# Optimization experiments

Hardware: AMD Instinct MI355X
Metric: run time of the kernel (lower is better)

The kernel has to match this reference:

```python
import jax, jax.numpy as jnp
import numpy as np

N_TOPICS = 1024
TOPIC_DIM = 128
HIDDEN = 512
N_HEADS = 8
HEAD_DIM = HIDDEN // N_HEADS
N_LAYERS = 2
ALPHA = 0.2
TIME_DECAY = 0.1
BATCH = 8


def setup_inputs() -> dict:
    key = jax.random.key(0)
    ks = jax.random.split(key, 16)
    inp = {
        'topic_ids': jax.random.randint(ks[0], (BATCH,), 0, N_TOPICS, dtype=jnp.int32),
        'adj_matrix': jax.random.randint(ks[1], (BATCH, N_TOPICS, N_TOPICS), 0, 2, dtype=jnp.int32),
        'time_matrix': jax.random.uniform(ks[2], (BATCH, N_TOPICS, N_TOPICS), dtype=jnp.float32),
        'attractiveness': jax.random.normal(ks[3], (BATCH,), dtype=jnp.float32),
        # parameters (torch Linear convention: W [out,in], y = x@W.T + b)
        'topic_embedding': jax.random.normal(ks[4], (N_TOPICS, TOPIC_DIM), dtype=jnp.float32) * 0.1,
        'struct_W': jax.random.normal(ks[5], (HIDDEN, TOPIC_DIM), dtype=jnp.float32) * 0.05,
        'struct_b': jnp.zeros((HIDDEN,), dtype=jnp.float32),
        'attract_W': jax.random.normal(ks[6], (HIDDEN, 1), dtype=jnp.float32) * 0.05,
        'attract_b': jnp.zeros((HIDDEN,), dtype=jnp.float32),
        'gat_W': jax.random.normal(ks[7], (N_LAYERS, N_HEADS, HIDDEN, HEAD_DIM), dtype=jnp.float32) * 0.05,
        'gat_a': jax.random.normal(ks[8], (N_LAYERS, N_HEADS, 2 * HEAD_DIM, 1), dtype=jnp.float32) * 0.05,
        'fc1_W': jax.random.normal(ks[9], (HIDDEN, HIDDEN), dtype=jnp.float32) * 0.05,
        'fc1_b': jnp.zeros((HIDDEN,), dtype=jnp.float32),
        'fc2_W': jax.random.normal(ks[10], (1, HIDDEN), dtype=jnp.float32) * 0.05,
        'fc2_b': jnp.zeros((1,), dtype=jnp.float32),
    }
    return inp


def _gat_layer(node, adj, time_w, W, a):
    # node: [B,N,F], adj: [B,N,N] (0/1), time_w: [B,N,N]
    # W: [H,F,hd], a: [H,2*hd,1]
    h = jnp.einsum('bni,hio->bhno', node, W)  # [B,H,N,hd]
    # Additive attention: a = [a_src; a_dst] so e_ij = LeakyReLU(h_i.a_src + h_j.a_dst)
    a_src = a[:, :HEAD_DIM, 0]   # [H,hd]
    a_dst = a[:, HEAD_DIM:, 0]   # [H,hd]
    e_src = jnp.einsum('bhnd,hd->bhn', h, a_src)  # [B,H,N]
    e_dst = jnp.einsum('bhnd,hd->bhn', h, a_dst)  # [B,H,N]
    e = e_src[:, :, :, None] + e_dst[:, :, None, :]  # [B,H,N,N]
    e = jax.nn.leaky_relu(e, negative_slope=ALPHA)
    e = e * time_w[:, None, :, :]
    e = jnp.where(adj[:, None, :, :] == 0, -jnp.inf, e)
    attn = jax.nn.softmax(e, axis=-1)
    out = jnp.einsum('bhij,bhjd->bhid', attn, h)  # [B,H,N,hd]
    out = out.transpose(0, 2, 1, 3).reshape(node.shape[0], node.shape[1], -1)
    return jax.nn.elu(out)


def reference(topic_ids, adj_matrix, time_matrix, attractiveness,
              topic_embedding, struct_W, struct_b, attract_W, attract_b,
              gat_W, gat_a, fc1_W, fc1_b, fc2_W, fc2_b):
    # structural features for all topics -> hidden
    struct = topic_embedding @ struct_W.T + struct_b          # [N,hidden]
    attract = attractiveness[:, None] @ attract_W.T + attract_b  # [B,hidden]
    node = jnp.broadcast_to(struct[None], (BATCH, N_TOPICS, HIDDEN))
    # weighted co-occurrence time (eq.17)
    time_w = jnp.exp(-TIME_DECAY * (time_matrix.max() - time_matrix))  # [B,N,N]
    for l in range(N_LAYERS):
        node = _gat_layer(node, adj_matrix, time_w, gat_W[l], gat_a[l])
    # gather per-sample topic node feature
    topic_feat = jnp.take_along_axis(node, topic_ids[:, None, None].astype(jnp.int32), axis=1)[:, 0]  # [B,hidden]
    combined = topic_feat + attract
    hidden = jax.nn.relu(combined @ fc1_W.T + fc1_b)
    pred = hidden @ fc2_W.T + fc2_b  # [B,1]
    return pred
```

## Files before the change

### kernel.cpp

```cpp
#include <hip/hip_runtime.h>

#define NT 1024
#define TD 128
#define HID 512
#define NH 8
#define HD 64
#define NB 8

typedef unsigned short us;
typedef _Float16 h16;
typedef h16 half8 __attribute__((ext_vector_type(8)));
typedef h16 h16x2 __attribute__((ext_vector_type(2)));
typedef float f32x4 __attribute__((ext_vector_type(4)));

#define LOG2E 1.44269504f

extern "C" __device__ _Float16 __ocml_exp2_f16(_Float16);

__device__ __forceinline__ us f2h(float x) { return __builtin_bit_cast(us, (h16)x); }
__device__ __forceinline__ float h2f(us s) { return (float)__builtin_bit_cast(h16, s); }
__device__ __forceinline__ unsigned int pkh2(float a, float b) {
    auto v = __builtin_amdgcn_cvt_pkrtz(a, b);
    return __builtin_bit_cast(unsigned int, v);
}

__global__ __launch_bounds__(256) void kprep(const float* __restrict__ tm, float* __restrict__ part,
                                             const float* __restrict__ emb, const float* __restrict__ sW,
                                             const float* __restrict__ sb, us* __restrict__ node0b,
                                             const float* __restrict__ gW, us* __restrict__ Wt,
                                             const float* __restrict__ fc2b, float* __restrict__ out) {
    __shared__ __align__(16) float smf[8768];
    int bx = blockIdx.x, t = threadIdx.x;
    if (bx < 1024) {
        const float4* tm4 = (const float4*)tm;
        size_t base = (size_t)bx * 256 + t;
        float m = -1e30f;
        #pragma unroll
        for (int k = 0; k < 8; k++) {
            float4 v = tm4[base + (size_t)k * 262144];
            m = fmaxf(m, fmaxf(fmaxf(v.x, v.y), fmaxf(v.z, v.w)));
        }
        smf[t] = m; __syncthreads();
        for (int s = 128; s > 0; s >>= 1) { if (t < s) smf[t] = fmaxf(smf[t], smf[t + s]); __syncthreads(); }
        if (t == 0) part[bx] = smf[0];
    } else if (bx < 1152) {
        int g = bx - 1024; int iblk = g & 15, oseg = g >> 4;
        us* As = (us*)smf;
        us* Bs = (us*)smf + 64 * 136;
        const float4* esrc = (const float4*)(emb + (size_t)iblk * 64 * TD);
        const float4* wsrc = (const float4*)(sW + (size_t)oseg * 64 * TD);
        #pragma unroll
        for (int rep = 0; rep < 8; rep++) {
            int f = rep * 256 + t;
            int row = f >> 5, c4 = f & 31;
            float4 av = esrc[f];
            float4 bv = wsrc[f];
            uint2 pa, pb;
            pa.x = pkh2(av.x, av.y); pa.y = pkh2(av.z, av.w);
            pb.x = pkh2(bv.x, bv.y); pb.y = pkh2(bv.z, bv.w);
            *(uint2*)&As[row * 136 + c4 * 4] = pa;
            *(uint2*)&Bs[row * 136 + c4 * 4] = pb;
        }
        __syncthreads();
        int l = t & 63, w = t >> 6, m = l & 15, q = l >> 4;
        f32x4 acc[4];
        #pragma unroll
        for (int ot = 0; ot < 4; ot++) acc[ot] = (f32x4){0.f, 0.f, 0.f, 0.f};
        #pragma unroll
        for (int ks = 0; ks < 4; ks++) {
            half8 a = *(const half8*)&As[(w * 16 + m) * 136 + ks * 32 + q * 8];
            #pragma unroll
            for (int ot = 0; ot < 4; ot++) {
                half8 b = *(const half8*)&Bs[(ot * 16 + m) * 136 + ks * 32 + q * 8];
                acc[ot] = __builtin_amdgcn_mfma_f32_16x16x32_f16(a, b, acc[ot], 0, 0, 0);
            }
        }
        #pragma unroll
        for (int ot = 0; ot < 4; ot++) {
            int col = oseg * 64 + ot * 16 + m;
            float sbv = sb[col];
            #pragma unroll
            for (int rr = 0; rr < 4; rr++) {
                int rowi = iblk * 64 + w * 16 + q * 4 + rr;
                node0b[(size_t)rowi * HID + col] = f2h(acc[ot][rr] + sbv);
            }
        }
    } else {
        int g = bx - 1152; int lh = g >> 3, kt = g & 7;
        if (g == 0 && t < NB) out[t] = fc2b[0];
        float* tile = smf;
        const float4* src = (const float4*)(gW + ((size_t)lh * HID + kt * 64) * HD);
        #pragma unroll
        for (int rep = 0; rep < 4; rep++) {
            int f = rep * 256 + t;
            float4 v = src[f];
            int row = f >> 4, col = (f & 15) * 4;
            float* d = tile + row * 65 + col;
            d[0] = v.x; d[1] = v.y; d[2] = v.z; d[3] = v.w;
        }
        __syncthreads();
        int o = t >> 2, ks = (t & 3) * 16;
        us pk[16];
        #pragma unroll
        for (int j = 0; j < 16; j++) pk[j] = f2h(tile[(ks + j) * 65 + o]);
        us* dst = Wt + (size_t)lh * HD * HID + (size_t)o * HID + kt * 64 + ks;
        *(uint4*)dst = *(uint4*)pk;
        *(uint4*)(dst + 8) = *(uint4*)&pk[8];
    }
}

__device__ __forceinline__ void gemm_body(const us* __restrict__ A, const us* __restrict__ W,
                                          const float* __restrict__ gav,
                                          us* __restrict__ outT, us* __restrict__ outR,
                                          float* __restrict__ esO, float* __restrict__ edO,
                                          int iblk, int b, int h, int t, us* sm) {
    us* As = sm;
    us* Bs = sm + 2 * 4608;
    int row = t >> 2, ks = t & 3;
    int l = t & 63, w = t >> 6, m = l & 15, q = l >> 4;
    size_t arow0 = (size_t)(b * NT + iblk * 64);
    const us* ar = A + (arow0 + row) * HID + ks * 16;
    const us* br = W + ((size_t)(h * HD + row)) * HID + ks * 16;
    f32x4 acc[4];
    #pragma unroll
    for (int ot = 0; ot < 4; ot++) acc[ot] = (f32x4){0.f, 0.f, 0.f, 0.f};
    {
        uint4 x0 = *(const uint4*)ar, x1 = *(const uint4*)(ar + 8);
        uint4 y0 = *(const uint4*)br, y1 = *(const uint4*)(br + 8);
        *(uint4*)&As[row * 72 + ks * 16] = x0; *(uint4*)&As[row * 72 + ks * 16 + 8] = x1;
        *(uint4*)&Bs[row * 72 + ks * 16] = y0; *(uint4*)&Bs[row * 72 + ks * 16 + 8] = y1;
    }
    uint4 a0 = *(const uint4*)(ar + 64), a1 = *(const uint4*)(ar + 72);
    uint4 b0 = *(const uint4*)(br + 64), b1 = *(const uint4*)(br + 72);
    for (int it = 0; it < 8; it++) {
        int cur = it & 1, nxt = cur ^ 1;
        uint4 na0, na1, nb0, nb1;
        if (it < 6) {
            int k0 = (it + 2) * 64;
            na0 = *(const uint4*)(ar + k0); na1 = *(const uint4*)(ar + k0 + 8);
            nb0 = *(const uint4*)(br + k0); nb1 = *(const uint4*)(br + k0 + 8);
        }
        __syncthreads();
        if (it < 7) {
            *(uint4*)&As[nxt * 4608 + row * 72 + ks * 16] = a0;
            *(uint4*)&As[nxt * 4608 + row * 72 + ks * 16 + 8] = a1;
            *(uint4*)&Bs[nxt * 4608 + row * 72 + ks * 16] = b0;
            *(uint4*)&Bs[nxt * 4608 + row * 72 + ks * 16 + 8] = b1;
        }
        const us* Ac = As + cur * 4608; const us* Bc = Bs + cur * 4608;
        #pragma unroll
        for (int kt = 0; kt < 2; kt++) {
            half8 av = *(const half8*)&Ac[(w * 16 + m) * 72 + kt * 32 + q * 8];
            #pragma unroll
            for (int ot = 0; ot < 4; ot++) {
                half8 bv = *(const half8*)&Bc[(ot * 16 + m) * 72 + kt * 32 + q * 8];
                acc[ot] = __builtin_amdgcn_mfma_f32_16x16x32_f16(av, bv, acc[ot], 0, 0, 0);
            }
        }
        if (it < 6) { a0 = na0; a1 = na1; b0 = nb0; b1 = nb1; }
    }
    const float* gas = gav + h * 2 * HD;
    float gs[4], gd[4];
    #pragma unroll
    for (int ot = 0; ot < 4; ot++) { gs[ot] = gas[ot * 16 + m]; gd[ot] = gas[HD + ot * 16 + m]; }
    size_t ebase = ((size_t)b * NH + h) * NT + iblk * 64;
    #pragma unroll
    for (int rr = 0; rr < 4; rr++) {
        float s = 0.f, d = 0.f;
        #pragma unroll
        for (int ot = 0; ot < 4; ot++) { float v = acc[ot][rr]; s = fmaf(v, gs[ot], s); d = fmaf(v, gd[ot], d); }
        #pragma unroll
        for (int mask = 1; mask < 16; mask <<= 1) { s += __shfl_xor(s, mask); d += __shfl_xor(d, mask); }
        if (m == 0) {
            int rowi = w * 16 + q * 4 + rr;
            esO[ebase + rowi] = s;
            edO[ebase + rowi] = d;
        }
    }
    #pragma unroll
    for (int ot = 0; ot < 4; ot++) {
        int col = h * HD + ot * 16 + m;
        #pragma unroll
        for (int rr = 0; rr < 4; rr++) {
            int i_loc = w * 16 + q * 4 + rr;
            float v = acc[ot][rr];
            if (outT) outT[(size_t)col * NT + iblk * 64 + i_loc] = f2h(v);
            if (outR) outR[(arow0 + i_loc) * HID + col] = f2h(v);
        }
    }
}

__global__ __launch_bounds__(256) void kphase1(const float* __restrict__ tm, const int* __restrict__ adj,
                                               const float* __restrict__ part, us* __restrict__ TWb,
                                               const us* __restrict__ node0b, const us* __restrict__ Wt,
                                               const float* __restrict__ ga, us* __restrict__ Ht1,
                                               float* __restrict__ es1, float* __restrict__ ed1) {
    __shared__ __align__(16) us sm[4 * 4608];
    int bx = blockIdx.x, t = threadIdx.x;
    if (bx < 2048) {
        float* red = (float*)sm;
        float m = fmaxf(fmaxf(part[t * 4], part[t * 4 + 1]), fmaxf(part[t * 4 + 2], part[t * 4 + 3]));
        red[t] = m; __syncthreads();
        for (int s = 128; s > 0; s >>= 1) { if (t < s) red[t] = fmaxf(red[t], red[t + s]); __syncthreads(); }
        float tmx = red[0];
        const float C = 0.1f * LOG2E;
        const float NANF = __uint_as_float(0x7FC00000u);
        #pragma unroll
        for (int it = 0; it < 4; it++) {
            size_t idx = (((size_t)bx * 4 + it) * 256 + t) * 4;
            float4 tv = *(const float4*)(tm + idx);
            int4 av = *(const int4*)(adj + idx);
            float w0 = exp2f((tv.x - tmx) * C) * LOG2E;
            float w1 = exp2f((tv.y - tmx) * C) * LOG2E;
            float w2 = exp2f((tv.z - tmx) * C) * LOG2E;
            float w3 = exp2f((tv.w - tmx) * C) * LOG2E;
            w0 = av.x ? w0 : NANF;
            w1 = av.y ? w1 : NANF;
            w2 = av.z ? w2 : NANF;
            w3 = av.w ? w3 : NANF;
            uint2 pk;
            pk.x = pkh2(w0, w1);
            pk.y = pkh2(w2, w3);
            *(uint2*)&TWb[idx] = pk;
        }
    } else {
        int g = bx - 2048;
        gemm_body(node0b, Wt, ga, Ht1, nullptr, es1, ed1, g & 15, 0, g >> 4, t, sm);
    }
}

__global__ __launch_bounds__(256) void kedge(const float* __restrict__ es, const float* __restrict__ ed,
                                             us* __restrict__ E1) {
    int g = blockIdx.x;
    int h = g >> 8, i0 = (g & 255) << 2;
    int t = threadIdx.x;
    __shared__ float eds[NT];
    *(float4*)&eds[t * 4] = *(const float4*)&ed[h * NT + t * 4];
    __syncthreads();
    int j = t * 4;
    float4 e4 = *(const float4*)&eds[j];
    #pragma unroll
    for (int r = 0; r < 4; r++) {
        float esv = es[h * NT + i0 + r];
        float a = esv + e4.x; a = fmaxf(a, 0.2f * a);
        float bq = esv + e4.y; bq = fmaxf(bq, 0.2f * bq);
        float c = esv + e4.z; c = fmaxf(c, 0.2f * c);
        float d = esv + e4.w; d = fmaxf(d, 0.2f * d);
        uint2 pk;
        pk.x = pkh2(a, bq);
        pk.y = pkh2(c, d);
        *(uint2*)&E1[((size_t)(h * NT) + i0 + r) * NT + j] = pk;
    }
}

__global__ __launch_bounds__(256) void kgemm2(const us* __restrict__ node1b, const us* __restrict__ Wt2,
                                              const float* __restrict__ ga2, us* __restrict__ H2b,
                                              float* __restrict__ es2, float* __restrict__ ed2) {
    __shared__ __align__(16) us sm[4 * 4608];
    int x = blockIdx.x;
    gemm_body(node1b, Wt2, ga2, nullptr, H2b, es2, ed2, x & 15, x >> 4, blockIdx.y, threadIdx.x, sm);
}

__device__ __forceinline__ unsigned int p_word(unsigned int tw, unsigned int ev) {
    h16x2 t = __builtin_bit_cast(h16x2, tw);
    h16x2 e = __builtin_bit_cast(h16x2, ev);
    h16x2 m = t * e;
    h16x2 p;
    p.x = __ocml_exp2_f16(m.x);
    p.y = __ocml_exp2_f16(m.y);
    h16x2 z = {(h16)0.0f, (h16)0.0f};
    h16x2 r = __builtin_elementwise_max(p, z);
    return __builtin_bit_cast(unsigned int, r);
}

__device__ __forceinline__ void compute_p(uint4 T0, uint4 T1, uint4 E0, uint4 E1v,
                                          uint4& P01, uint4& P23) {
    P01.x = p_word(T0.x, E0.x);
    P01.y = p_word(T0.y, E0.y);
    P01.z = p_word(T0.z, E0.z);
    P01.w = p_word(T0.w, E0.w);
    P23.x = p_word(T1.x, E1v.x);
    P23.y = p_word(T1.y, E1v.y);
    P23.z = p_word(T1.z, E1v.z);
    P23.w = p_word(T1.w, E1v.w);
}

__global__ __launch_bounds__(256) void kattn1(const us* __restrict__ TWb, const us* __restrict__ Ht,
                                              const us* __restrict__ E1, us* __restrict__ node1b) {
    int x = blockIdx.x; int iblk = x & 15; int b = x >> 4; int h = blockIdx.y;
    int t = threadIdx.x;
    __shared__ __align__(16) us Ps[2 * 4608];
    __shared__ __align__(16) us Hs[2 * 4608];
    __shared__ float invl_s[64];
    int i = t >> 2, js = t & 3;
    int l = t & 63, w = t >> 6, m = l & 15, q = l >> 4;
    const us* twrow = TWb + ((size_t)(b * NT) + iblk * 64 + i) * NT + js * 16;
    const us* erow  = E1 + ((size_t)(h * NT) + iblk * 64 + i) * NT + js * 16;
    const us* htrow = Ht + ((size_t)(h * HD) + i) * NT + js * 16;
    f32x4 acc[4];
    #pragma unroll
    for (int ot = 0; ot < 4; ot++) acc[ot] = (f32x4){0.f, 0.f, 0.f, 0.f};
    f32x4 acc1 = (f32x4){0.f, 0.f, 0.f, 0.f};
    h16 ov = (m == 0) ? (h16)1.0f : (h16)0.0f;
    half8 bones = {ov, ov, ov, ov, ov, ov, ov, ov};
    uint4 T0, T1, E0, E1r, Hh0, Hh1;
    T0 = *(const uint4*)twrow; T1 = *(const uint4*)(twrow + 8);
    E0 = *(const uint4*)erow;  E1r = *(const uint4*)(erow + 8);
    Hh0 = *(const uint4*)htrow; Hh1 = *(const uint4*)(htrow + 8);
    {
        uint4 p01, p23;
        compute_p(T0, T1, E0, E1r, p01, p23);
        us* Pd = Ps + i * 72 + js * 16;
        us* Hd = Hs + i * 72 + js * 16;
        *(uint4*)Pd = p01; *(uint4*)(Pd + 8) = p23;
        *(uint4*)Hd = Hh0; *(uint4*)(Hd + 8) = Hh1;
    }
    T0 = *(const uint4*)(twrow + 64); T1 = *(const uint4*)(twrow + 72);
    E0 = *(const uint4*)(erow + 64);  E1r = *(const uint4*)(erow + 72);
    Hh0 = *(const uint4*)(htrow + 64); Hh1 = *(const uint4*)(htrow + 72);
    for (int it = 0; it < 16; it++) {
        int cur = it & 1, nxt = cur ^ 1;
        uint4 nT0, nT1, nE0, nE1, nH0, nH1;
        if (it < 14) {
            int j0 = (it + 2) * 64;
            nT0 = *(const uint4*)(twrow + j0); nT1 = *(const uint4*)(twrow + j0 + 8);
            nE0 = *(const uint4*)(erow + j0);  nE1 = *(const uint4*)(erow + j0 + 8);
            nH0 = *(const uint4*)(htrow + j0); nH1 = *(const uint4*)(htrow + j0 + 8);
        }
        uint4 p01, p23;
        if (it < 15) compute_p(T0, T1, E0, E1r, p01, p23);
        __syncthreads();
        if (it < 15) {
            us* Pd = Ps + nxt * 4608 + i * 72 + js * 16;
            us* Hd = Hs + nxt * 4608 + i * 72 + js * 16;
            *(uint4*)Pd = p01; *(uint4*)(Pd + 8) = p23;
            *(uint4*)Hd = Hh0; *(uint4*)(Hd + 8) = Hh1;
        }
        const us* Pc = Ps + cur * 4608; const us* Hc = Hs + cur * 4608;
        #pragma unroll
        for (int kt = 0; kt < 2; kt++) {
            half8 av = *(const half8*)&Pc[(w * 16 + m) * 72 + kt * 32 + q * 8];
            #pragma unroll
            for (int ot = 0; ot < 4; ot++) {
                half8 bv = *(const half8*)&Hc[(ot * 16 + m) * 72 + kt * 32 + q * 8];
                acc[ot] = __builtin_amdgcn_mfma_f32_16x16x32_f16(av, bv, acc[ot], 0, 0, 0);
            }
            acc1 = __builtin_amdgcn_mfma_f32_16x16x32_f16(av, bones, acc1, 0, 0, 0);
        }
        if (it < 14) { T0 = nT0; T1 = nT1; E0 = nE0; E1r = nE1; Hh0 = nH0; Hh1 = nH1; }
    }
    if (m == 0) {
        #pragma unroll
        for (int rr = 0; rr < 4; rr++) invl_s[w * 16 + q * 4 + rr] = 1.f / acc1[rr];
    }
    __syncthreads();
    #pragma unroll
    for (int ot = 0; ot < 4; ot++) {
        int col = h * HD + ot * 16 + m;
        #pragma unroll
        for (int rr = 0; rr < 4; rr++) {
            int i_loc = w * 16 + q * 4 + rr;
            float v = acc[ot][rr] * invl_s[i_loc];
            v = v > 0.f ? v : (__expf(v) - 1.f);
            node1b[(size_t)(b * NT + iblk * 64 + i_loc) * HID + col] = f2h(v);
        }
    }
}

__global__ __launch_bounds__(256) void kattn2a(const us* __restrict__ TWb, const us* __restrict__ H2b,
                                               const float* __restrict__ es2, const float* __restrict__ ed2,
                                               const int* __restrict__ topic_ids,
                                               float* __restrict__ ppv, float* __restrict__ pl) {
    int js = blockIdx.x, h = blockIdx.y, b = blockIdx.z;
    int t = threadIdx.x;
    __shared__ float pls[64];
    __shared__ float red[256];
    int qi = topic_ids[b];
    if (t < 64) {
        int j = js * 64 + t;
        float esq = es2[((size_t)b * NH + h) * NT + qi];
        float tw = h2f(TWb[((size_t)(b * NT) + qi) * NT + j]);
        float e = esq + ed2[((size_t)b * NH + h) * NT + j];
        e = fmaxf(e, 0.2f * e) * tw;
        float p = fmaxf(exp2f(e), 0.f);
        pls[t] = p;
        float lsum = p;
        #pragma unroll
        for (int mask = 1; mask < 64; mask <<= 1) lsum += __shfl_xor(lsum, mask);
        if (t == 0) pl[((size_t)b * NH + h) * 16 + js] = lsum;
    }
    __syncthreads();
    int o = t & 63, jg = t >> 6;
    float acc = 0.f;
    const us* hb = H2b + ((size_t)(b * NT) + js * 64 + jg * 16) * HID + h * HD + o;
    #pragma unroll
    for (int jj = 0; jj < 16; jj++)
        acc = fmaf(pls[jg * 16 + jj], h2f(hb[(size_t)jj * HID]), acc);
    red[t] = acc; __syncthreads();
    if (t < 64) {
        float pv = red[t] + red[t + 64] + red[t + 128] + red[t + 192];
        ppv[(((size_t)b * NH + h) * 16 + js) * HD + t] = pv;
    }
}

__global__ __launch_bounds__(256) void khead2(const float* __restrict__ ppv, const float* __restrict__ pl,
                                              const float* __restrict__ attr,
                                              const float* __restrict__ aW, const float* __restrict__ ab,
                                              const float* __restrict__ fc1W, const float* __restrict__ fc1b,
                                              const float* __restrict__ fc2W, float* __restrict__ out) {
    int kseg = blockIdx.x, b = blockIdx.y;
    int t = threadIdx.x;
    __shared__ float comb[HID];
    __shared__ float linv[NH];
    __shared__ float r2[256];
    if (t < NH) {
        float lsum = 0.f;
        #pragma unroll
        for (int js = 0; js < 16; js++) lsum += pl[((size_t)b * NH + t) * 16 + js];
        linv[t] = 1.f / lsum;
    }
    __syncthreads();
    float av = attr[b];
    for (int k = t; k < HID; k += 256) {
        int h = k >> 6, o = k & 63;
        float pv = 0.f;
        #pragma unroll
        for (int js = 0; js < 16; js++) pv += ppv[(((size_t)b * NH + h) * 16 + js) * HD + o];
        float v = pv * linv[h];
        v = v > 0.f ? v : (__expf(v) - 1.f);
        comb[k] = v + av * aW[k] + ab[k];
    }
    __syncthreads();
    int kk = kseg * 16 + (t >> 4);
    int j = t & 15;
    const float* row = fc1W + (size_t)kk * HID;
    float acc = 0.f;
    #pragma unroll 8
    for (int mi = 0; mi < 32; mi++) {
        int idx = mi * 16 + j;
        acc = fmaf(comb[idx], row[idx], acc);
    }
    #pragma unroll
    for (int mask = 1; mask < 16; mask <<= 1) acc += __shfl_xor(acc, mask);
    float partv = 0.f;
    if (j == 0) {
        float hk = fmaxf(acc + fc1b[kk], 0.f);
        partv = hk * fc2W[kk];
    }
    r2[t] = partv; __syncthreads();
    for (int s = 128; s > 0; s >>= 1) { if (t < s) r2[t] += r2[t + s]; __syncthreads(); }
    if (t == 0) atomicAdd(&out[b], r2[0]);
}

extern "C" void kernel_launch(void* const* d_in, const int* in_sizes, int n_in,
                              void* d_out, int out_size, void* d_ws, size_t ws_size,
                              hipStream_t stream) {
    const int*   topic_ids = (const int*)d_in[0];
    const int*   adj       = (const int*)d_in[1];
    const float* tm        = (const float*)d_in[2];
    const float* attr      = (const float*)d_in[3];
    const float* emb       = (const float*)d_in[4];
    const float* sW        = (const float*)d_in[5];
    const float* sb        = (const float*)d_in[6];
    const float* aW        = (const float*)d_in[7];
    const float* ab        = (const float*)d_in[8];
    const float* gW        = (const float*)d_in[9];
    const float* ga        = (const float*)d_in[10];
    const float* fc1W      = (const float*)d_in[11];
    const float* fc1b      = (const float*)d_in[12];
    const float* fc2W      = (const float*)d_in[13];
    const float* fc2b      = (const float*)d_in[14];
    float* out = (float*)d_out;

    char* p = (char*)d_ws;
    us* TWb    = (us*)p; p += sizeof(us) * (size_t)NB * NT * NT;
    us* E1     = (us*)p; p += sizeof(us) * (size_t)NH * NT * NT;
    us* node0b = (us*)p; p += sizeof(us) * (size_t)NT * HID;
    us* Wt     = (us*)p; p += sizeof(us) * (size_t)2 * NH * HD * HID;
    us* Ht1    = (us*)p; p += sizeof(us) * (size_t)HID * NT;
    us* node1b = (us*)p; p += sizeof(us) * (size_t)NB * NT * HID;
    us* H2b    = (us*)p; p += sizeof(us) * (size_t)NB * NT * HID;
    float* es1  = (float*)p; p += sizeof(float) * NH * NT;
    float* ed1  = (float*)p; p += sizeof(float) * NH * NT;
    float* es2  = (float*)p; p += sizeof(float) * NB * NH * NT;
    float* ed2  = (float*)p; p += sizeof(float) * NB * NH * NT;
    float* ppv  = (float*)p; p += sizeof(float) * NB * NH * 16 * HD;
    float* pl   = (float*)p; p += sizeof(float) * NB * NH * 16;
    float* part = (float*)p; p += sizeof(float) * 1024;

    kprep<<<1280, 256, 0, stream>>>(tm, part, emb, sW, sb, node0b, gW, Wt, fc2b, out);
    kphase1<<<2176, 256, 0, stream>>>(tm, adj, part, TWb, node0b, Wt, ga, Ht1, es1, ed1);
    kedge<<<2048, 256, 0, stream>>>(es1, ed1, E1);
    kattn1<<<dim3(16 * NB, NH), 256, 0, stream>>>(TWb, Ht1, E1, node1b);
    kgemm2<<<dim3(16 * NB, NH), 256, 0, stream>>>(node1b, Wt + (size_t)NH * HD * HID,
                                                  ga + NH * 2 * HD, H2b, es2, ed2);
    kattn2a<<<dim3(16, NH, NB), 256, 0, stream>>>(TWb, H2b, es2, ed2, topic_ids, ppv, pl);
    khead2<<<dim3(32, NB), 256, 0, stream>>>(ppv, pl, attr, aW, ab, fc1W, fc1b, fc2W, out);
}
```

Baseline: 193.6 us.

## Fuse edge-score computation into layer-1 attention and drop precomputed E1 matrix

Removes the kedge kernel that materialized an H×N×N fp16 edge-score matrix, and instead computes leaky_relu(es_i + ed_j) on the fly inside kattn1 from a shared-memory copy of ed and a per-row es value. This eliminates a 16 MB write plus its reread per attention block. The grid is also flattened to 1D with batch as the fastest-varying index, so blocks sharing the same head's Ht and E data are co-scheduled for cache reuse. In exchange, the addition and leaky-relu move to fp16 arithmetic in the inner loop, which costs a little ALU work and slightly changes precision.

```diff
diff --git a/kernel.cpp b/kernel.cpp
--- a/kernel.cpp
+++ b/kernel.cpp
@@ -229,73 +229,63 @@
     }
 }
 
-__global__ __launch_bounds__(256) void kedge(const float* __restrict__ es, const float* __restrict__ ed,
-                                             us* __restrict__ E1) {
-    int g = blockIdx.x;
-    int h = g >> 8, i0 = (g & 255) << 2;
-    int t = threadIdx.x;
-    __shared__ float eds[NT];
-    *(float4*)&eds[t * 4] = *(const float4*)&ed[h * NT + t * 4];
-    __syncthreads();
-    int j = t * 4;
-    float4 e4 = *(const float4*)&eds[j];
-    #pragma unroll
-    for (int r = 0; r < 4; r++) {
-        float esv = es[h * NT + i0 + r];
-        float a = esv + e4.x; a = fmaxf(a, 0.2f * a);
-        float bq = esv + e4.y; bq = fmaxf(bq, 0.2f * bq);
-        float c = esv + e4.z; c = fmaxf(c, 0.2f * c);
-        float d = esv + e4.w; d = fmaxf(d, 0.2f * d);
-        uint2 pk;
-        pk.x = pkh2(a, bq);
-        pk.y = pkh2(c, d);
-        *(uint2*)&E1[((size_t)(h * NT) + i0 + r) * NT + j] = pk;
-    }
-}
-
 __global__ __launch_bounds__(256) void kgemm2(const us* __restrict__ node1b, const us* __restrict__ Wt2,
                                               const float* __restrict__ ga2, us* __restrict__ H2b,
                                               float* __restrict__ es2, float* __restrict__ ed2) {
     __shared__ __align__(16) us sm[4 * 4608];
-    int x = blockIdx.x;
-    gemm_body(node1b, Wt2, ga2, nullptr, H2b, es2, ed2, x & 15, x >> 4, blockIdx.y, threadIdx.x, sm);
-}
-
-__device__ __forceinline__ unsigned int p_word(unsigned int tw, unsigned int ev) {
+    int n = blockIdx.x;
+    int b = n & 7, k = n >> 3, iblk = k & 15, h = k >> 4;
+    gemm_body(node1b, Wt2, ga2, nullptr, H2b, es2, ed2, iblk, b, h, threadIdx.x, sm);
+}
+
+__device__ __forceinline__ unsigned int p_word_fly(unsigned int tw, unsigned int ed, h16x2 es) {
     h16x2 t = __builtin_bit_cast(h16x2, tw);
-    h16x2 e = __builtin_bit_cast(h16x2, ev);
-    h16x2 m = t * e;
+    h16x2 d = __builtin_bit_cast(h16x2, ed);
+    h16x2 e = es + d;
+    h16x2 lk = e * (h16)0.2f;
+    h16x2 el = __builtin_elementwise_max(e, lk);
+    h16x2 mm = t * el;
     h16x2 p;
-    p.x = __ocml_exp2_f16(m.x);
-    p.y = __ocml_exp2_f16(m.y);
+    p.x = __ocml_exp2_f16(mm.x);
+    p.y = __ocml_exp2_f16(mm.y);
     h16x2 z = {(h16)0.0f, (h16)0.0f};
     h16x2 r = __builtin_elementwise_max(p, z);
     return __builtin_bit_cast(unsigned int, r);
 }
 
-__device__ __forceinline__ void compute_p(uint4 T0, uint4 T1, uint4 E0, uint4 E1v,
-                                          uint4& P01, uint4& P23) {
-    P01.x = p_word(T0.x, E0.x);
-    P01.y = p_word(T0.y, E0.y);
-    P01.z = p_word(T0.z, E0.z);
-    P01.w = p_word(T0.w, E0.w);
-    P23.x = p_word(T1.x, E1v.x);
-    P23.y = p_word(T1.y, E1v.y);
-    P23.z = p_word(T1.z, E1v.z);
-    P23.w = p_word(T1.w, E1v.w);
+__device__ __forceinline__ void compute_p_fly(uint4 T0, uint4 T1, uint4 D0, uint4 D1, h16x2 es,
+                                              uint4& P01, uint4& P23) {
+    P01.x = p_word_fly(T0.x, D0.x, es);
+    P01.y = p_word_fly(T0.y, D0.y, es);
+    P01.z = p_word_fly(T0.z, D0.z, es);
+    P01.w = p_word_fly(T0.w, D0.w, es);
+    P23.x = p_word_fly(T1.x, D1.x, es);
+    P23.y = p_word_fly(T1.y, D1.y, es);
+    P23.z = p_word_fly(T1.z, D1.z, es);
+    P23.w = p_word_fly(T1.w, D1.w, es);
 }
 
 __global__ __launch_bounds__(256) void kattn1(const us* __restrict__ TWb, const us* __restrict__ Ht,
-                                              const us* __restrict__ E1, us* __restrict__ node1b) {
-    int x = blockIdx.x; int iblk = x & 15; int b = x >> 4; int h = blockIdx.y;
+                                              const float* __restrict__ es1, const float* __restrict__ ed1,
+                                              us* __restrict__ node1b) {
+    int n = blockIdx.x;
+    int b = n & 7, k = n >> 3, iblk = k & 15, h = k >> 4;
     int t = threadIdx.x;
     __shared__ __align__(16) us Ps[2 * 4608];
     __shared__ __align__(16) us Hs[2 * 4608];
+    __shared__ __align__(16) us edl[NT];
     __shared__ float invl_s[64];
     int i = t >> 2, js = t & 3;
     int l = t & 63, w = t >> 6, m = l & 15, q = l >> 4;
+    {
+        float4 ev = *(const float4*)&ed1[h * NT + t * 4];
+        uint2 pk; pk.x = pkh2(ev.x, ev.y); pk.y = pkh2(ev.z, ev.w);
+        *(uint2*)&edl[t * 4] = pk;
+    }
+    float esf = es1[h * NT + iblk * 64 + i];
+    h16 esh = (h16)esf;
+    h16x2 esv = {esh, esh};
     const us* twrow = TWb + ((size_t)(b * NT) + iblk * 64 + i) * NT + js * 16;
-    const us* erow  = E1 + ((size_t)(h * NT) + iblk * 64 + i) * NT + js * 16;
     const us* htrow = Ht + ((size_t)(h * HD) + i) * NT + js * 16;
     f32x4 acc[4];
     #pragma unroll
@@ -303,32 +293,37 @@
     f32x4 acc1 = (f32x4){0.f, 0.f, 0.f, 0.f};
     h16 ov = (m == 0) ? (h16)1.0f : (h16)0.0f;
     half8 bones = {ov, ov, ov, ov, ov, ov, ov, ov};
-    uint4 T0, T1, E0, E1r, Hh0, Hh1;
+    uint4 T0, T1, Hh0, Hh1;
     T0 = *(const uint4*)twrow; T1 = *(const uint4*)(twrow + 8);
-    E0 = *(const uint4*)erow;  E1r = *(const uint4*)(erow + 8);
     Hh0 = *(const uint4*)htrow; Hh1 = *(const uint4*)(htrow + 8);
+    __syncthreads();
     {
+        uint4 D0 = *(const uint4*)&edl[js * 16];
+        uint4 D1 = *(const uint4*)&edl[js * 16 + 8];
         uint4 p01, p23;
-        compute_p(T0, T1, E0, E1r, p01, p23);
+        compute_p_fly(T0, T1, D0, D1, esv, p01, p23);
         us* Pd = Ps + i * 72 + js * 16;
         us* Hd = Hs + i * 72 + js * 16;
         *(uint4*)Pd = p01; *(uint4*)(Pd + 8) = p23;
         *(uint4*)Hd = Hh0; *(uint4*)(Hd + 8) = Hh1;
     }
     T0 = *(const uint4*)(twrow + 64); T1 = *(const uint4*)(twrow + 72);
-    E0 = *(const uint4*)(erow + 64);  E1r = *(const uint4*)(erow + 72);
     Hh0 = *(const uint4*)(htrow + 64); Hh1 = *(const uint4*)(htrow + 72);
     for (int it = 0; it < 16; it++) {
         int cur = it & 1, nxt = cur ^ 1;
-        uint4 nT0, nT1, nE0, nE1, nH0, nH1;
+        uint4 nT0, nT1, nH0, nH1;
         if (it < 14) {
             int j0 = (it + 2) * 64;
             nT0 = *(const uint4*)(twrow + j0); nT1 = *(const uint4*)(twrow + j0 + 8);
-            nE0 = *(const uint4*)(erow + j0);  nE1 = *(const uint4*)(erow + j0 + 8);
             nH0 = *(const uint4*)(htrow + j0); nH1 = *(const uint4*)(htrow + j0 + 8);
         }
         uint4 p01, p23;
-        if (it < 15) compute_p(T0, T1, E0, E1r, p01, p23);
+        if (it < 15) {
+            int j0 = (it + 1) * 64;
+            uint4 D0 = *(const uint4*)&edl[j0 + js * 16];
+            uint4 D1 = *(const uint4*)&edl[j0 + js * 16 + 8];
+            compute_p_fly(T0, T1, D0, D1, esv, p01, p23);
+        }
         __syncthreads();
         if (it < 15) {
             us* Pd = Ps + nxt * 4608 + i * 72 + js * 16;
@@ -347,7 +342,7 @@
             }
             acc1 = __builtin_amdgcn_mfma_f32_16x16x32_f16(av, bones, acc1, 0, 0, 0);
         }
-        if (it < 14) { T0 = nT0; T1 = nT1; E0 = nE0; E1r = nE1; Hh0 = nH0; Hh1 = nH1; }
+        if (it < 14) { T0 = nT0; T1 = nT1; Hh0 = nH0; Hh1 = nH1; }
     }
     if (m == 0) {
         #pragma unroll
@@ -474,7 +469,6 @@
 
     char* p = (char*)d_ws;
     us* TWb    = (us*)p; p += sizeof(us) * (size_t)NB * NT * NT;
-    us* E1     = (us*)p; p += sizeof(us) * (size_t)NH * NT * NT;
     us* node0b = (us*)p; p += sizeof(us) * (size_t)NT * HID;
     us* Wt     = (us*)p; p += sizeof(us) * (size_t)2 * NH * HD * HID;
     us* Ht1    = (us*)p; p += sizeof(us) * (size_t)HID * NT;
@@ -490,10 +484,9 @@
 
     kprep<<<1280, 256, 0, stream>>>(tm, part, emb, sW, sb, node0b, gW, Wt, fc2b, out);
     kphase1<<<2176, 256, 0, stream>>>(tm, adj, part, TWb, node0b, Wt, ga, Ht1, es1, ed1);
-    kedge<<<2048, 256, 0, stream>>>(es1, ed1, E1);
-    kattn1<<<dim3(16 * NB, NH), 256, 0, stream>>>(TWb, Ht1, E1, node1b);
-    kgemm2<<<dim3(16 * NB, NH), 256, 0, stream>>>(node1b, Wt + (size_t)NH * HD * HID,
-                                                  ga + NH * 2 * HD, H2b, es2, ed2);
+    kattn1<<<1024, 256, 0, stream>>>(TWb, Ht1, es1, ed1, node1b);
+    kgemm2<<<1024, 256, 0, stream>>>(node1b, Wt + (size_t)NH * HD * HID,
+                                     ga + NH * 2 * HD, H2b, es2, ed2);
     kattn2a<<<dim3(16, NH, NB), 256, 0, stream>>>(TWb, H2b, es2, ed2, topic_ids, ppv, pl);
     khead2<<<dim3(32, NB), 256, 0, stream>>>(ppv, pl, attr, aW, ab, fc1W, fc1b, fc2W, out);
 }
```

Result: faster. 187.9 us (-2.9%).
